# Kernel tuning notes

Hardware: AMD Instinct MI355X
Metric: run time of the kernel (lower is better)

Reference implementation:

```python
import jax, jax.numpy as jnp
import numpy as np

H = 16          # num heads
HD = 64         # head dim
TEMPERATURE = 1.0
LN_EPS = 1e-5

def setup_inputs() -> dict:
    key = jax.random.key(0)
    ks = jax.random.split(key, 5)
    B, S, D = 2, 2048, 1024
    s = 1.0 / np.sqrt(D)
    return {
        "x": jax.random.normal(ks[0], (B, S, D), jnp.float32),
        "Wq": jax.random.normal(ks[1], (D, D), jnp.float32) * s,
        "bq": jnp.zeros((D,), jnp.float32),
        "Wk": jax.random.normal(ks[2], (D, D), jnp.float32) * s,
        "bk": jnp.zeros((D,), jnp.float32),
        "Wv": jax.random.normal(ks[3], (D, D), jnp.float32) * s,
        "bv": jnp.zeros((D,), jnp.float32),
        "Wo": jax.random.normal(ks[4], (D, D), jnp.float32) * s,
        "bo": jnp.zeros((D,), jnp.float32),
        "ln_gamma": jnp.ones((D,), jnp.float32),
        "ln_beta": jnp.zeros((D,), jnp.float32),
    }

def reference(x, Wq, bq, Wk, bk, Wv, bv, Wo, bo, ln_gamma, ln_beta):
    B, S, D = x.shape
    # LayerNorm (pre-attention)
    mu = jnp.mean(x, axis=-1, keepdims=True)
    var = jnp.mean(jnp.square(x - mu), axis=-1, keepdims=True)
    xn = (x - mu) * jax.lax.rsqrt(var + LN_EPS) * ln_gamma + ln_beta
    # Fused QKV projections (equivalent to H per-head Linears concatenated)
    q = (xn @ Wq + bq).reshape(B, S, H, HD)
    k = (xn @ Wk + bk).reshape(B, S, H, HD)
    v = (xn @ Wv + bv).reshape(B, S, H, HD)
    scale = np.sqrt(HD) * TEMPERATURE
    scores = jnp.einsum("bqhd,bkhd->bhqk", q, k) / scale
    attn = jax.nn.softmax(scores, axis=-1)  # dropout p=0 -> identity
    ctx = jnp.einsum("bhqk,bkhd->bqhd", attn, v).reshape(B, S, D)
    out = ctx @ Wo + bo
    return x + out
```

## Files before the change

kernel.cpp:

```cpp
#include <hip/hip_runtime.h>
#include <hip/hip_bf16.h>

#define Bc   2
#define Sc   2048
#define Dc   1024
#define Hc   16
#define HDc  64
#define MR   (Bc * Sc)
#define TBK  32
#define LOG2E 1.44269504088896f

typedef __attribute__((ext_vector_type(8))) short bf16x8;
typedef __attribute__((ext_vector_type(4))) float f32x4;
typedef __attribute__((ext_vector_type(4))) unsigned int u32x4;

__device__ __forceinline__ unsigned short f2bf(float f) {
    __hip_bfloat16 h = __float2bfloat16(f);
    return *reinterpret_cast<unsigned short*>(&h);
}

__device__ __forceinline__ void gll16(const unsigned short* g, unsigned short* l) {
    __builtin_amdgcn_global_load_lds(
        (__attribute__((address_space(1))) const unsigned int*)g,
        (__attribute__((address_space(3))) unsigned int*)l,
        16, 0, 0);
}

__global__ __launch_bounds__(256) void prep_kernel(
        const float* __restrict__ x, const float* __restrict__ gamma,
        const float* __restrict__ beta, unsigned short* __restrict__ xn,
        const float* __restrict__ W0, const float* __restrict__ W1,
        const float* __restrict__ W2, const float* __restrict__ W3,
        unsigned short* __restrict__ T0, unsigned short* __restrict__ T1,
        unsigned short* __restrict__ T2, unsigned short* __restrict__ T3) {
    __shared__ float tile[64][65];
    int idx = blockIdx.x;
    int t = threadIdx.x;

    if (idx < 1024) {
        int z = idx >> 8, rem = idx & 255;
        const float* W = (z == 0) ? W0 : (z == 1) ? W1 : (z == 2) ? W2 : W3;
        unsigned short* T = (z == 0) ? T0 : (z == 1) ? T1 : (z == 2) ? T2 : T3;
        int nb = (rem & 15) * 64, kb = (rem >> 4) * 64;
        int r0 = t >> 4, c4 = (t & 15) * 4;
        #pragma unroll
        for (int rr = 0; rr < 4; rr++) {
            int row = rr * 16 + r0;
            float4 v = *(const float4*)(W + (size_t)(kb + row) * Dc + nb + c4);
            tile[row][c4 + 0] = v.x; tile[row][c4 + 1] = v.y;
            tile[row][c4 + 2] = v.z; tile[row][c4 + 3] = v.w;
        }
        __syncthreads();
        #pragma unroll
        for (int rr = 0; rr < 4; rr++) {
            int nrow = rr * 16 + r0;
            ushort4 o;
            o.x = f2bf(tile[c4 + 0][nrow]); o.y = f2bf(tile[c4 + 1][nrow]);
            o.z = f2bf(tile[c4 + 2][nrow]); o.w = f2bf(tile[c4 + 3][nrow]);
            *(ushort4*)(T + (size_t)(nb + nrow) * Dc + kb + c4) = o;
        }
    } else {
        int row = idx - 1024;
        const float4* xr = (const float4*)(x + (size_t)row * Dc);
        float4 v = xr[t];
        float s  = v.x + v.y + v.z + v.w;
        float ss = v.x * v.x + v.y * v.y + v.z * v.z + v.w * v.w;
        #pragma unroll
        for (int off = 32; off; off >>= 1) {
            s  += __shfl_xor(s, off, 64);
            ss += __shfl_xor(ss, off, 64);
        }
        float* red = tile[0];
        int w = t >> 6, lane = t & 63;
        if (lane == 0) { red[w * 2] = s; red[w * 2 + 1] = ss; }
        __syncthreads();
        s  = red[0] + red[2] + red[4] + red[6];
        ss = red[1] + red[3] + red[5] + red[7];
        float mean = s * (1.0f / Dc);
        float var  = ss * (1.0f / Dc) - mean * mean;
        float rstd = rsqrtf(var + 1e-5f);
        float4 g = ((const float4*)gamma)[t], bb = ((const float4*)beta)[t];
        ushort4 o;
        o.x = f2bf((v.x - mean) * rstd * g.x + bb.x);
        o.y = f2bf((v.y - mean) * rstd * g.y + bb.y);
        o.z = f2bf((v.z - mean) * rstd * g.z + bb.z);
        o.w = f2bf((v.w - mean) * rstd * g.w + bb.w);
        *(ushort4*)(xn + (size_t)row * Dc + t * 4) = o;
    }
}

__device__ __forceinline__ void gemm_core(const unsigned short* __restrict__ A,
                                          const unsigned short* __restrict__ Wt,
                                          unsigned short* As, unsigned short* Bs,
                                          int m0, int n0, f32x4 acc[4][4]) {
    int t = threadIdx.x;
    int w = t >> 6, lane = t & 63;
    int l16 = lane & 15, quad = lane >> 4;
    int wm = (w >> 1) * 64, wn = (w & 1) * 64;

    int srow = lane >> 2;
    int scol = (lane & 3) * 8;
    const unsigned short* Ag = A  + (size_t)(m0 + w * 16 + srow) * Dc + scol;
    const unsigned short* Bg = Wt + (size_t)(n0 + w * 16 + srow) * Dc + scol;
    unsigned short* Asw = As + (w * 16) * TBK;
    unsigned short* Bsw = Bs + (w * 16) * TBK;

    for (int k0 = 0; k0 < Dc; k0 += TBK) {
        gll16(Ag + k0, Asw);
        gll16(Ag + k0 + (size_t)64 * Dc, Asw + 64 * TBK);
        gll16(Bg + k0, Bsw);
        gll16(Bg + k0 + (size_t)64 * Dc, Bsw + 64 * TBK);
        __syncthreads();
        bf16x8 af[4], bfr[4];
        #pragma unroll
        for (int i = 0; i < 4; i++) {
            af[i]  = *(const bf16x8*)(As + (wm + i * 16 + l16) * TBK + quad * 8);
            bfr[i] = *(const bf16x8*)(Bs + (wn + i * 16 + l16) * TBK + quad * 8);
        }
        #pragma unroll
        for (int i = 0; i < 4; i++)
            #pragma unroll
            for (int j = 0; j < 4; j++)
                acc[i][j] = __builtin_amdgcn_mfma_f32_16x16x32_bf16(af[i], bfr[j], acc[i][j], 0, 0, 0);
        __syncthreads();
    }
}

__global__ __launch_bounds__(256) void gemm_qkv_kernel(
        const unsigned short* __restrict__ A,
        const unsigned short* __restrict__ Wqt, const unsigned short* __restrict__ Wkt,
        const unsigned short* __restrict__ Wvt,
        const float* __restrict__ bq, const float* __restrict__ bk,
        const float* __restrict__ bv,
        unsigned short* __restrict__ Qb, unsigned short* __restrict__ Kb,
        unsigned short* __restrict__ Vtb) {
    __shared__ unsigned short As[128 * TBK];
    __shared__ unsigned short Bs[128 * TBK];
    int z = blockIdx.z;
    const unsigned short* Wt = (z == 0) ? Wqt : (z == 1) ? Wkt : Wvt;
    const float* bias = (z == 0) ? bq : (z == 1) ? bk : bv;
    unsigned short* Out = (z == 0) ? Qb : (z == 1) ? Kb : Vtb;
    float outscale = (z == 0) ? (0.125f * LOG2E) : 1.0f;

    int n0 = blockIdx.x * 128, m0 = blockIdx.y * 128;
    f32x4 acc[4][4];
    #pragma unroll
    for (int i = 0; i < 4; i++)
        #pragma unroll
        for (int j = 0; j < 4; j++) acc[i][j] = (f32x4){0.f, 0.f, 0.f, 0.f};

    gemm_core(A, Wt, As, Bs, m0, n0, acc);

    int t = threadIdx.x;
    int w = t >> 6, lane = t & 63;
    int l16 = lane & 15, quad = lane >> 4;
    int wm = (w >> 1) * 64, wn = (w & 1) * 64;
    int b = m0 >> 11;
    #pragma unroll
    for (int j = 0; j < 4; j++) {
        int col = n0 + wn + j * 16 + l16;
        float bb = bias[col];
        int h = col >> 6, d = col & 63;
        #pragma unroll
        for (int i = 0; i < 4; i++) {
            #pragma unroll
            for (int r = 0; r < 4; r++) {
                int row = m0 + wm + i * 16 + quad * 4 + r;
                int s = row & (Sc - 1);
                unsigned short v = f2bf((acc[i][j][r] + bb) * outscale);
                if (z != 2)
                    Out[(((size_t)(b * Hc + h)) * Sc + s) * HDc + d] = v;
                else
                    Out[(((size_t)(b * Hc + h)) * HDc + d) * Sc + s] = v;
            }
        }
    }
}

__global__ __launch_bounds__(256) void gemm_o_kernel(
        const unsigned short* __restrict__ A,
        const unsigned short* __restrict__ Wot,
        const float* __restrict__ bo, const float* __restrict__ resid,
        float* __restrict__ Out) {
    __shared__ unsigned short As[128 * TBK];
    __shared__ unsigned short Bs[128 * TBK];
    int n0 = blockIdx.x * 128, m0 = blockIdx.y * 128;

    f32x4 acc[4][4];
    #pragma unroll
    for (int i = 0; i < 4; i++)
        #pragma unroll
        for (int j = 0; j < 4; j++) acc[i][j] = (f32x4){0.f, 0.f, 0.f, 0.f};

    gemm_core(A, Wot, As, Bs, m0, n0, acc);

    int t = threadIdx.x;
    int w = t >> 6, lane = t & 63;
    int l16 = lane & 15, quad = lane >> 4;
    int wm = (w >> 1) * 64, wn = (w & 1) * 64;
    #pragma unroll
    for (int j = 0; j < 4; j++) {
        int col = n0 + wn + j * 16 + l16;
        float bb = bo[col];
        #pragma unroll
        for (int i = 0; i < 4; i++) {
            #pragma unroll
            for (int r = 0; r < 4; r++) {
                int row = m0 + wm + i * 16 + quad * 4 + r;
                size_t off = (size_t)row * Dc + col;
                Out[off] = acc[i][j][r] + bb + resid[off];
            }
        }
    }
}

#define BKa 64

__global__ __launch_bounds__(256, 2) void attn_mfma_kernel(
        const unsigned short* __restrict__ Q,
        const unsigned short* __restrict__ K,
        const unsigned short* __restrict__ Vt,
        unsigned short* __restrict__ O) {
    __shared__ unsigned short Ks[BKa * 64];
    __shared__ unsigned short Vs[HDc * 64];

    int t = threadIdx.x;
    int w = t >> 6, lane = t & 63;
    int quad = lane >> 4, l16 = lane & 15;

    int bid = blockIdx.x + gridDim.x * blockIdx.y;
    int q0 = (bid >> 5) * 128;
    int bh = bid & 31;
    size_t qkbase = (size_t)bh * Sc * HDc;
    size_t vbase  = (size_t)bh * HDc * Sc;

    bf16x8 qf[2][2];
    #pragma unroll
    for (int jq = 0; jq < 2; jq++) {
        const unsigned short* qr = Q + qkbase
            + (size_t)(q0 + w * 32 + jq * 16 + l16) * HDc + quad * 8;
        qf[jq][0] = *(const bf16x8*)(qr);
        qf[jq][1] = *(const bf16x8*)(qr + 32);
    }

    f32x4 Oacc[2][4];
    #pragma unroll
    for (int jq = 0; jq < 2; jq++)
        #pragma unroll
        for (int n = 0; n < 4; n++) Oacc[jq][n] = (f32x4){0.f, 0.f, 0.f, 0.f};
    float lacc[2] = {0.f, 0.f};

    int srow = t >> 2, sseg = t & 3;
    const unsigned short* Kg = K + qkbase + (size_t)srow * HDc + sseg * 16;
    const unsigned short* Vg = Vt + vbase + (size_t)srow * Sc + sseg * 16;
    int rk = srow & 7;
    unsigned short* ksw0 = Ks + srow * 64 + ((2 * sseg)     ^ rk) * 8;
    unsigned short* ksw1 = Ks + srow * 64 + ((2 * sseg + 1) ^ rk) * 8;
    unsigned short* vsw0 = Vs + srow * 64 + ((2 * sseg)     ^ rk) * 8;
    unsigned short* vsw1 = Vs + srow * 64 + ((2 * sseg + 1) ^ rk) * 8;
    int rm = l16 & 7;
    const int NT = Sc / BKa;

    bf16x8 kv0 = *(const bf16x8*)(Kg);
    bf16x8 kv1 = *(const bf16x8*)(Kg + 8);
    bf16x8 vv0 = *(const bf16x8*)(Vg);
    bf16x8 vv1 = *(const bf16x8*)(Vg + 8);

    for (int kt = 0; kt < NT; kt++) {
        __syncthreads();
        *(bf16x8*)(ksw0) = kv0;
        *(bf16x8*)(ksw1) = kv1;
        *(bf16x8*)(vsw0) = vv0;
        *(bf16x8*)(vsw1) = vv1;
        __syncthreads();

        int ktn = (kt + 1 < NT) ? kt + 1 : kt;
        const unsigned short* kgn = Kg + (size_t)ktn * BKa * HDc;
        const unsigned short* vgn = Vg + ktn * BKa;
        kv0 = *(const bf16x8*)(kgn);
        kv1 = *(const bf16x8*)(kgn + 8);
        vv0 = *(const bf16x8*)(vgn);
        vv1 = *(const bf16x8*)(vgn + 8);

        f32x4 st[2][4];
        __builtin_amdgcn_s_setprio(1);
        #pragma unroll
        for (int m = 0; m < 4; m++) {
            const unsigned short* kr = Ks + (m * 16 + l16) * 64;
            bf16x8 kf0 = *(const bf16x8*)(kr + ((quad)     ^ rm) * 8);
            bf16x8 kf1 = *(const bf16x8*)(kr + ((quad + 4) ^ rm) * 8);
            #pragma unroll
            for (int jq = 0; jq < 2; jq++) {
                f32x4 s = (f32x4){0.f, 0.f, 0.f, 0.f};
                s = __builtin_amdgcn_mfma_f32_16x16x32_bf16(kf0, qf[jq][0], s, 0, 0, 0);
                s = __builtin_amdgcn_mfma_f32_16x16x32_bf16(kf1, qf[jq][1], s, 0, 0, 0);
                st[jq][m] = s;
            }
        }
        __builtin_amdgcn_s_setprio(0);

        u32x4 pa[2][2];
        #pragma unroll
        for (int jq = 0; jq < 2; jq++) {
            float e[4][4];
            #pragma unroll
            for (int m = 0; m < 4; m++) {
                e[m][0] = __builtin_amdgcn_exp2f(st[jq][m][0]);
                e[m][1] = __builtin_amdgcn_exp2f(st[jq][m][1]);
                e[m][2] = __builtin_amdgcn_exp2f(st[jq][m][2]);
                e[m][3] = __builtin_amdgcn_exp2f(st[jq][m][3]);
                lacc[jq] += (e[m][0] + e[m][1]) + (e[m][2] + e[m][3]);
            }
            #pragma unroll
            for (int kk = 0; kk < 2; kk++) {
                unsigned int A, B, C, D;
                asm("v_cvt_pk_bf16_f32 %0, %1, %2"
                    : "=v"(A) : "v"(e[2 * kk][0]), "v"(e[2 * kk][1]));
                asm("v_cvt_pk_bf16_f32 %0, %1, %2"
                    : "=v"(B) : "v"(e[2 * kk][2]), "v"(e[2 * kk][3]));
                asm("v_cvt_pk_bf16_f32 %0, %1, %2"
                    : "=v"(C) : "v"(e[2 * kk + 1][0]), "v"(e[2 * kk + 1][1]));
                asm("v_cvt_pk_bf16_f32 %0, %1, %2"
                    : "=v"(D) : "v"(e[2 * kk + 1][2]), "v"(e[2 * kk + 1][3]));
                asm("v_permlane32_swap_b32 %0, %1" : "+v"(A), "+v"(C));
                asm("v_permlane32_swap_b32 %0, %1" : "+v"(B), "+v"(D));
                asm("v_permlane16_swap_b32 %0, %1" : "+v"(A), "+v"(C));
                asm("v_permlane16_swap_b32 %0, %1" : "+v"(B), "+v"(D));
                pa[jq][kk] = (u32x4){A, B, C, D};
            }
        }

        __builtin_amdgcn_s_setprio(1);
        #pragma unroll
        for (int kk = 0; kk < 2; kk++) {
            bf16x8 vf[4];
            #pragma unroll
            for (int n = 0; n < 4; n++)
                vf[n] = *(const bf16x8*)(Vs + (n * 16 + l16) * 64
                                         + ((4 * kk + quad) ^ rm) * 8);
            #pragma unroll
            for (int jq = 0; jq < 2; jq++) {
                bf16x8 pf = *reinterpret_cast<const bf16x8*>(&pa[jq][kk]);
                #pragma unroll
                for (int n = 0; n < 4; n++)
                    Oacc[jq][n] = __builtin_amdgcn_mfma_f32_16x16x32_bf16(pf, vf[n], Oacc[jq][n], 0, 0, 0);
            }
        }
        __builtin_amdgcn_s_setprio(0);
    }

    int b = bh >> 4, h = bh & 15;
    #pragma unroll
    for (int jq = 0; jq < 2; jq++) {
        lacc[jq] += __shfl_xor(lacc[jq], 16, 64);
        lacc[jq] += __shfl_xor(lacc[jq], 32, 64);
        #pragma unroll
        for (int i = 0; i < 4; i++) {
            float li = __shfl(lacc[jq], quad * 4 + i, 64);
            float rl = 1.0f / li;
            int q = q0 + w * 32 + jq * 16 + quad * 4 + i;
            #pragma unroll
            for (int n = 0; n < 4; n++) {
                O[((size_t)(b * Sc + q)) * Dc + h * HDc + n * 16 + l16] =
                    f2bf(Oacc[jq][n][i] * rl);
            }
        }
    }
}

extern "C" void kernel_launch(void* const* d_in, const int* in_sizes, int n_in,
                              void* d_out, int out_size, void* d_ws, size_t ws_size,
                              hipStream_t stream) {
    const float* x     = (const float*)d_in[0];
    const float* Wq    = (const float*)d_in[1];
    const float* bq    = (const float*)d_in[2];
    const float* Wk    = (const float*)d_in[3];
    const float* bk    = (const float*)d_in[4];
    const float* Wv    = (const float*)d_in[5];
    const float* bv    = (const float*)d_in[6];
    const float* Wo    = (const float*)d_in[7];
    const float* bo    = (const float*)d_in[8];
    const float* gamma = (const float*)d_in[9];
    const float* beta  = (const float*)d_in[10];
    float* out = (float*)d_out;

    unsigned short* us = (unsigned short*)d_ws;
    const size_t NE = (size_t)MR * Dc;
    const size_t WE = (size_t)Dc * Dc;
    unsigned short* xn  = us;
    unsigned short* Qb  = us + NE;
    unsigned short* Kb  = us + 2 * NE;
    unsigned short* Vtb = us + 3 * NE;
    unsigned short* ctx = us + 4 * NE;
    unsigned short* Wqt = us + 5 * NE;
    unsigned short* Wkt = Wqt + WE;
    unsigned short* Wvt = Wkt + WE;
    unsigned short* Wot = Wvt + WE;

    prep_kernel<<<1024 + MR, 256, 0, stream>>>(x, gamma, beta, xn,
                                               Wq, Wk, Wv, Wo,
                                               Wqt, Wkt, Wvt, Wot);

    dim3 qkvgrid(Dc / 128, MR / 128, 3);
    gemm_qkv_kernel<<<qkvgrid, 256, 0, stream>>>(xn, Wqt, Wkt, Wvt, bq, bk, bv,
                                                 Qb, Kb, Vtb);

    dim3 agrid(Sc / 128, Bc * Hc);
    attn_mfma_kernel<<<agrid, 256, 0, stream>>>(Qb, Kb, Vtb, ctx);

    dim3 ogrid(Dc / 128, MR / 128);
    gemm_o_kernel<<<ogrid, 256, 0, stream>>>(ctx, Wot, bo, x, out);
}
```

Baseline: 201.2 us.

## Halve attention query tile and compute row sums with MFMA against ones

Each attention block now handles 64 queries (16 per wave) instead of 128, doubling the grid and raising the occupancy target to 4 blocks per CU. The softmax denominator is accumulated by an extra MFMA of the probability tile against a ones vector, which replaces the scalar adds and cross-lane shuffles. This should improve latency hiding and cut VALU work. In exchange, K/V tiles are loaded and staged through LDS twice as often per query, and the row sums now come from bf16-rounded probabilities.

```diff
diff --git a/kernel.cpp b/kernel.cpp
--- a/kernel.cpp
+++ b/kernel.cpp
@@ -216,7 +216,7 @@
 
 #define BKa 64
 
-__global__ __launch_bounds__(256, 2) void attn_mfma_kernel(
+__global__ __launch_bounds__(256, 4) void attn_mfma_kernel(
         const unsigned short* __restrict__ Q,
         const unsigned short* __restrict__ K,
         const unsigned short* __restrict__ Vt,
@@ -229,26 +229,24 @@
     int quad = lane >> 4, l16 = lane & 15;
 
     int bid = blockIdx.x + gridDim.x * blockIdx.y;
-    int q0 = (bid >> 5) * 128;
+    int q0 = (bid >> 5) * 64;
     int bh = bid & 31;
     size_t qkbase = (size_t)bh * Sc * HDc;
     size_t vbase  = (size_t)bh * HDc * Sc;
 
-    bf16x8 qf[2][2];
-    #pragma unroll
-    for (int jq = 0; jq < 2; jq++) {
-        const unsigned short* qr = Q + qkbase
-            + (size_t)(q0 + w * 32 + jq * 16 + l16) * HDc + quad * 8;
-        qf[jq][0] = *(const bf16x8*)(qr);
-        qf[jq][1] = *(const bf16x8*)(qr + 32);
-    }
-
-    f32x4 Oacc[2][4];
-    #pragma unroll
-    for (int jq = 0; jq < 2; jq++)
-        #pragma unroll
-        for (int n = 0; n < 4; n++) Oacc[jq][n] = (f32x4){0.f, 0.f, 0.f, 0.f};
-    float lacc[2] = {0.f, 0.f};
+    const unsigned short* qr = Q + qkbase
+        + (size_t)(q0 + w * 16 + l16) * HDc + quad * 8;
+    bf16x8 qf0 = *(const bf16x8*)(qr);
+    bf16x8 qf1 = *(const bf16x8*)(qr + 32);
+
+    f32x4 Oacc[4];
+    #pragma unroll
+    for (int n = 0; n < 4; n++) Oacc[n] = (f32x4){0.f, 0.f, 0.f, 0.f};
+    f32x4 Lacc = (f32x4){0.f, 0.f, 0.f, 0.f};
+
+    bf16x8 ones;
+    #pragma unroll
+    for (int i = 0; i < 8; i++) ones[i] = (short)0x3F80;
 
     int srow = t >> 2, sseg = t & 3;
     const unsigned short* Kg = K + qkbase + (size_t)srow * HDc + sseg * 16;
@@ -282,88 +280,71 @@
         vv0 = *(const bf16x8*)(vgn);
         vv1 = *(const bf16x8*)(vgn + 8);
 
-        f32x4 st[2][4];
+        f32x4 st[4];
         __builtin_amdgcn_s_setprio(1);
         #pragma unroll
         for (int m = 0; m < 4; m++) {
             const unsigned short* kr = Ks + (m * 16 + l16) * 64;
             bf16x8 kf0 = *(const bf16x8*)(kr + ((quad)     ^ rm) * 8);
             bf16x8 kf1 = *(const bf16x8*)(kr + ((quad + 4) ^ rm) * 8);
-            #pragma unroll
-            for (int jq = 0; jq < 2; jq++) {
-                f32x4 s = (f32x4){0.f, 0.f, 0.f, 0.f};
-                s = __builtin_amdgcn_mfma_f32_16x16x32_bf16(kf0, qf[jq][0], s, 0, 0, 0);
-                s = __builtin_amdgcn_mfma_f32_16x16x32_bf16(kf1, qf[jq][1], s, 0, 0, 0);
-                st[jq][m] = s;
-            }
+            f32x4 s = (f32x4){0.f, 0.f, 0.f, 0.f};
+            s = __builtin_amdgcn_mfma_f32_16x16x32_bf16(kf0, qf0, s, 0, 0, 0);
+            s = __builtin_amdgcn_mfma_f32_16x16x32_bf16(kf1, qf1, s, 0, 0, 0);
+            st[m] = s;
         }
         __builtin_amdgcn_s_setprio(0);
 
-        u32x4 pa[2][2];
-        #pragma unroll
-        for (int jq = 0; jq < 2; jq++) {
-            float e[4][4];
-            #pragma unroll
-            for (int m = 0; m < 4; m++) {
-                e[m][0] = __builtin_amdgcn_exp2f(st[jq][m][0]);
-                e[m][1] = __builtin_amdgcn_exp2f(st[jq][m][1]);
-                e[m][2] = __builtin_amdgcn_exp2f(st[jq][m][2]);
-                e[m][3] = __builtin_amdgcn_exp2f(st[jq][m][3]);
-                lacc[jq] += (e[m][0] + e[m][1]) + (e[m][2] + e[m][3]);
-            }
-            #pragma unroll
-            for (int kk = 0; kk < 2; kk++) {
-                unsigned int A, B, C, D;
-                asm("v_cvt_pk_bf16_f32 %0, %1, %2"
-                    : "=v"(A) : "v"(e[2 * kk][0]), "v"(e[2 * kk][1]));
-                asm("v_cvt_pk_bf16_f32 %0, %1, %2"
-                    : "=v"(B) : "v"(e[2 * kk][2]), "v"(e[2 * kk][3]));
-                asm("v_cvt_pk_bf16_f32 %0, %1, %2"
-                    : "=v"(C) : "v"(e[2 * kk + 1][0]), "v"(e[2 * kk + 1][1]));
-                asm("v_cvt_pk_bf16_f32 %0, %1, %2"
-                    : "=v"(D) : "v"(e[2 * kk + 1][2]), "v"(e[2 * kk + 1][3]));
-                asm("v_permlane32_swap_b32 %0, %1" : "+v"(A), "+v"(C));
-                asm("v_permlane32_swap_b32 %0, %1" : "+v"(B), "+v"(D));
-                asm("v_permlane16_swap_b32 %0, %1" : "+v"(A), "+v"(C));
-                asm("v_permlane16_swap_b32 %0, %1" : "+v"(B), "+v"(D));
-                pa[jq][kk] = (u32x4){A, B, C, D};
-            }
+        float e[4][4];
+        #pragma unroll
+        for (int m = 0; m < 4; m++) {
+            e[m][0] = __builtin_amdgcn_exp2f(st[m][0]);
+            e[m][1] = __builtin_amdgcn_exp2f(st[m][1]);
+            e[m][2] = __builtin_amdgcn_exp2f(st[m][2]);
+            e[m][3] = __builtin_amdgcn_exp2f(st[m][3]);
+        }
+        u32x4 pa[2];
+        #pragma unroll
+        for (int kk = 0; kk < 2; kk++) {
+            unsigned int A, B, C, D;
+            asm("v_cvt_pk_bf16_f32 %0, %1, %2"
+                : "=v"(A) : "v"(e[2 * kk][0]), "v"(e[2 * kk][1]));
+            asm("v_cvt_pk_bf16_f32 %0, %1, %2"
+                : "=v"(B) : "v"(e[2 * kk][2]), "v"(e[2 * kk][3]));
+            asm("v_cvt_pk_bf16_f32 %0, %1, %2"
+                : "=v"(C) : "v"(e[2 * kk + 1][0]), "v"(e[2 * kk + 1][1]));
+            asm("v_cvt_pk_bf16_f32 %0, %1, %2"
+                : "=v"(D) : "v"(e[2 * kk + 1][2]), "v"(e[2 * kk + 1][3]));
+            asm("v_permlane32_swap_b32 %0, %1" : "+v"(A), "+v"(C));
+            asm("v_permlane32_swap_b32 %0, %1" : "+v"(B), "+v"(D));
+            asm("v_permlane16_swap_b32 %0, %1" : "+v"(A), "+v"(C));
+            asm("v_permlane16_swap_b32 %0, %1" : "+v"(B), "+v"(D));
+            pa[kk] = (u32x4){A, B, C, D};
         }
 
         __builtin_amdgcn_s_setprio(1);
         #pragma unroll
         for (int kk = 0; kk < 2; kk++) {
-            bf16x8 vf[4];
-            #pragma unroll
-            for (int n = 0; n < 4; n++)
-                vf[n] = *(const bf16x8*)(Vs + (n * 16 + l16) * 64
-                                         + ((4 * kk + quad) ^ rm) * 8);
-            #pragma unroll
-            for (int jq = 0; jq < 2; jq++) {
-                bf16x8 pf = *reinterpret_cast<const bf16x8*>(&pa[jq][kk]);
-                #pragma unroll
-                for (int n = 0; n < 4; n++)
-                    Oacc[jq][n] = __builtin_amdgcn_mfma_f32_16x16x32_bf16(pf, vf[n], Oacc[jq][n], 0, 0, 0);
-            }
-        }
-        __builtin_amdgcn_s_setprio(0);
-    }
-
-    int b = bh >> 4, h = bh & 15;
-    #pragma unroll
-    for (int jq = 0; jq < 2; jq++) {
-        lacc[jq] += __shfl_xor(lacc[jq], 16, 64);
-        lacc[jq] += __shfl_xor(lacc[jq], 32, 64);
-        #pragma unroll
-        for (int i = 0; i < 4; i++) {
-            float li = __shfl(lacc[jq], quad * 4 + i, 64);
-            float rl = 1.0f / li;
-            int q = q0 + w * 32 + jq * 16 + quad * 4 + i;
+            bf16x8 pf = *reinterpret_cast<const bf16x8*>(&pa[kk]);
             #pragma unroll
             for (int n = 0; n < 4; n++) {
-                O[((size_t)(b * Sc + q)) * Dc + h * HDc + n * 16 + l16] =
-                    f2bf(Oacc[jq][n][i] * rl);
+                bf16x8 vf = *(const bf16x8*)(Vs + (n * 16 + l16) * 64
+                                             + ((4 * kk + quad) ^ rm) * 8);
+                Oacc[n] = __builtin_amdgcn_mfma_f32_16x16x32_bf16(pf, vf, Oacc[n], 0, 0, 0);
             }
+            Lacc = __builtin_amdgcn_mfma_f32_16x16x32_bf16(pf, ones, Lacc, 0, 0, 0);
+        }
+        __builtin_amdgcn_s_setprio(0);
+    }
+
+    int b = bh >> 4, h = bh & 15;
+    #pragma unroll
+    for (int i = 0; i < 4; i++) {
+        float rl = 1.0f / Lacc[i];
+        int q = q0 + w * 16 + quad * 4 + i;
+        #pragma unroll
+        for (int n = 0; n < 4; n++) {
+            O[((size_t)(b * Sc + q)) * Dc + h * HDc + n * 16 + l16] =
+                f2bf(Oacc[n][i] * rl);
         }
     }
 }
@@ -405,7 +386,7 @@
     gemm_qkv_kernel<<<qkvgrid, 256, 0, stream>>>(xn, Wqt, Wkt, Wvt, bq, bk, bv,
                                                  Qb, Kb, Vtb);
 
-    dim3 agrid(Sc / 128, Bc * Hc);
+    dim3 agrid(Sc / 64, Bc * Hc);
     attn_mfma_kernel<<<agrid, 256, 0, stream>>>(Qb, Kb, Vtb, ctx);
 
     dim3 ogrid(Dc / 128, MR / 128);
```

Measured after the change: 204.2 us. About the same (+1.5%).
